# Kernel tuning notes

Measured on AMD Instinct MI355X. Metric: run time of the kernel, lower is better.

The kernel has to match this reference:

```python
import jax, jax.numpy as jnp
import numpy as np

B = 2048
S = 8            # mem_slots
H = 8            # num_heads
HS = 128         # head_size
KS = 128         # key_size (= head_size)
VS = 128         # value_size
M = H * HS       # mem_size = 1024
QKV = 2 * KS + VS            # 384
TOTAL = QKV * H              # 3072
IN_DIM = 1024
NUM_GATES = 2                # gate_style='memory' -> gate size 1, x2 gates
FORGET_BIAS = 1.0
INPUT_BIAS = 0.0


def _glorot(key, shape):
    fan_in, fan_out = shape[0], shape[1]
    lim = np.sqrt(6.0 / (fan_in + fan_out))
    return jax.random.uniform(key, shape, jnp.float32, -lim, lim)


def setup_inputs() -> dict:
    key = jax.random.key(0)
    ks = jax.random.split(key, 16)
    return {
        "inputs": jax.random.normal(ks[0], (B, IN_DIM), jnp.float32),
        "memory": jax.random.normal(ks[1], (B, S * M), jnp.float32),
        "kernel_qkv": _glorot(ks[2], (M, TOTAL)),
        "bias_qkv": jnp.zeros((TOTAL,), jnp.float32),
        "kernel_gi": _glorot(ks[3], (M, NUM_GATES)),
        "bias_gi": _glorot(ks[4], (1, NUM_GATES))[0],
        "kernel_gm": _glorot(ks[5], (M, NUM_GATES)),
        "bias_gm": _glorot(ks[6], (1, NUM_GATES))[0],
        "kernel_in": _glorot(ks[7], (IN_DIM, M)),
        "bias_in": _glorot(ks[8], (1, M))[0],
        "mlp_k0": _glorot(ks[9], (M, M)),
        "mlp_b0": _glorot(ks[10], (1, M))[0],
        "mlp_k1": _glorot(ks[11], (M, M)),
        "mlp_b1": _glorot(ks[12], (1, M))[0],
    }


def reference(inputs, memory, kernel_qkv, bias_qkv, kernel_gi, bias_gi,
              kernel_gm, bias_gm, kernel_in, bias_in,
              mlp_k0, mlp_b0, mlp_k1, mlp_b1):
    b = inputs.shape[0]
    mem = memory.reshape(b, S, M)                       # (B, S, M)
    x = inputs @ kernel_in + bias_in                    # (B, M)
    mpi = jnp.concatenate([mem, x[:, None, :]], axis=1)  # (B, S+1, M)

    # multi-head attention over memory + input slot
    qkv = (mpi @ kernel_qkv + bias_qkv).reshape(b, S + 1, H, QKV)
    qkv = qkv.transpose(0, 2, 1, 3)                     # (B, H, S+1, QKV)
    q = qkv[..., :KS] * (QKV ** -0.5)
    k = qkv[..., KS:2 * KS]
    v = qkv[..., 2 * KS:]
    w = jax.nn.softmax(jnp.einsum('bhqd,bhkd->bhqk', q, k), axis=-1)
    att = jnp.einsum('bhqk,bhkd->bhqd', w, v)           # (B, H, S+1, VS)
    att = att.transpose(0, 2, 1, 3).reshape(b, S + 1, M)
    m1 = mpi + att                                      # residual attention

    # residual 2-layer MLP (relu between layers)
    h = jax.nn.relu(m1 @ mlp_k0 + mlp_b0)
    m2 = m1 + (h @ mlp_k1 + mlp_b1)

    nxt = m2[:, :-1, :]                                 # drop input slot

    # per-slot (memory-style) gates
    gi = (x @ kernel_gi + bias_gi)[:, None, :]          # (B, 1, 2)
    gm = jnp.tanh(mem) @ kernel_gm + bias_gm            # (B, S, 2)
    gates = gm + gi
    input_gate = jax.nn.sigmoid(gates[..., :1] + INPUT_BIAS)
    forget_gate = jax.nn.sigmoid(gates[..., 1:] + FORGET_BIAS)

    nxt = input_gate * jnp.tanh(nxt) + forget_gate * mem
    return nxt.reshape(b, S * M)
```

## Files before the change

kernel.cpp:

```cpp
#include <hip/hip_runtime.h>
#include <math.h>


typedef unsigned short ushort_t;
typedef short bf16x8_t __attribute__((ext_vector_type(8)));
typedef float f32x4_t  __attribute__((ext_vector_type(4)));

#define MFMA16(a, b, c) __builtin_amdgcn_mfma_f32_16x16x32_bf16((a), (b), (c), 0, 0, 0)

__device__ __forceinline__ ushort_t f2bf(float f) {
    unsigned int u = __float_as_uint(f);
    u += 0x7fff + ((u >> 16) & 1);
    return (ushort_t)(u >> 16);
}
__device__ __forceinline__ float bf2f(ushort_t h) {
    return __uint_as_float(((unsigned int)h) << 16);
}
__device__ __forceinline__ float fast_tanh(float x) {
    float e = __expf(2.0f * x);
    return 1.0f - 2.0f * __builtin_amdgcn_rcpf(e + 1.0f);
}
__device__ __forceinline__ float fast_sigmoid(float x) {
    return __builtin_amdgcn_rcpf(1.0f + __expf(-x));
}

__device__ __forceinline__ void load_lds_16(const void* g, void* l) {
    __builtin_amdgcn_global_load_lds(
        (const __attribute__((address_space(1))) void*)g,
        (__attribute__((address_space(3))) void*)l, 16, 0, 0);
}

__global__ __launch_bounds__(256)
void gemm128db(const ushort_t* __restrict__ A, const ushort_t* __restrict__ Wt,
               const float* __restrict__ bias, float* __restrict__ Cf,
               ushort_t* __restrict__ Cb, const ushort_t* __restrict__ resb,
               const float* __restrict__ igfg, const ushort_t* __restrict__ memb,
               float* __restrict__ outp, int N, int K, int relu,
               int ncol, int nrow)
{
    __shared__ __align__(16) ushort_t As[2][128][32];
    __shared__ __align__(16) ushort_t Bs[2][128][32];
    const int tid  = threadIdx.x;
    const int wave = tid >> 6, lane = tid & 63;
    const int wr = (wave >> 1) * 64;
    const int wc = (wave & 1)  * 64;
    const int lrow  = lane & 15;
    const int lquad = lane >> 4;

    int l = blockIdx.x, rT, cT;
    if ((nrow & 7) == 0) {
        int group = l / (8 * ncol);
        int w     = l - group * 8 * ncol;
        rT = group * 8 + (w & 7);
        cT = w >> 3;
    } else {
        rT = l / ncol;
        cT = l - rT * ncol;
    }
    const int rowBase = rT * 128;
    const int colBase = cT * 128;

    auto stage = [&](const ushort_t* __restrict__ G, int gbase, int k0,
                     ushort_t (*lds)[32]) {
        #pragma unroll
        for (int i = 0; i < 2; ++i) {
            int e   = i * 256 + tid;
            int row = e >> 2;
            int sl  = e & 3;
            int gc  = sl ^ ((row >> 1) & 3);
            const ushort_t* g = G + (size_t)(gbase + row) * K + k0 + gc * 8;
            load_lds_16(g, &lds[row][sl * 8]);
        }
    };

    f32x4_t acc[4][4] = {};

    stage(A,  rowBase, 0, As[0]);
    stage(Wt, colBase, 0, Bs[0]);
    __syncthreads();

    int buf = 0;
    for (int k0 = 0; k0 < K; k0 += 32) {
        if (k0 + 32 < K) {
            stage(A,  rowBase, k0 + 32, As[buf ^ 1]);
            stage(Wt, colBase, k0 + 32, Bs[buf ^ 1]);
        }

        bf16x8_t af[4], bfr[4];
        #pragma unroll
        for (int t = 0; t < 4; ++t) {
            int ma = wr + t * 16 + lrow;
            int pa = lquad ^ ((ma >> 1) & 3);
            af[t]  = *(const bf16x8_t*)&As[buf][ma][pa * 8];
            int nb = wc + t * 16 + lrow;
            int pb = lquad ^ ((nb >> 1) & 3);
            bfr[t] = *(const bf16x8_t*)&Bs[buf][nb][pb * 8];
        }
        #pragma unroll
        for (int mi = 0; mi < 4; ++mi)
            #pragma unroll
            for (int ni = 0; ni < 4; ++ni)
                acc[mi][ni] = MFMA16(af[mi], bfr[ni], acc[mi][ni]);

        __syncthreads();
        buf ^= 1;
    }

    #pragma unroll
    for (int mi = 0; mi < 4; ++mi) {
        #pragma unroll
        for (int ni = 0; ni < 4; ++ni) {
            int col = colBase + wc + ni * 16 + lrow;
            float bv = bias[col];
            #pragma unroll
            for (int r = 0; r < 4; ++r) {
                int row = rowBase + wr + mi * 16 + lquad * 4 + r;
                size_t idx = (size_t)row * N + col;
                float v = acc[mi][ni][r] + bv;
                if (resb) v += bf2f(resb[idx]);
                if (relu) v = fmaxf(v, 0.f);
                if (outp) {
                    float ig = igfg[row * 2], fg = igfg[row * 2 + 1];
                    float mv = bf2f(memb[(size_t)(row + (row >> 3)) * N + col]);
                    outp[idx] = ig * fast_tanh(v) + fg * mv;
                } else if (Cb) {
                    Cb[idx] = f2bf(v);
                } else {
                    Cf[idx] = v;
                }
            }
        }
    }
}

__global__ __launch_bounds__(512, 2)
void gemm256(const ushort_t* __restrict__ A, const ushort_t* __restrict__ Wt,
             const float* __restrict__ bias, ushort_t* __restrict__ Cb,
             int N, int K, int ncol, int nrow)
{
    __shared__ __align__(16) ushort_t As[2][256][64];
    __shared__ __align__(16) ushort_t Bs[2][256][64];

    const int tid   = threadIdx.x;
    const int wave  = tid >> 6, lane = tid & 63;
    const int lrow  = lane & 15, lquad = lane >> 4;
    const int wr    = (wave >> 2) * 64;
    const int wc    = (wave & 3) * 32;

    const int nwg = ncol * nrow;
    int l = blockIdx.x;
    int q = nwg >> 3, r = nwg & 7;
    int xcd = l & 7, ib = l >> 3;
    int wg = (xcd < r) ? xcd * (q + 1) + ib : r * (q + 1) + (xcd - r) * q + ib;
    int rT = wg / ncol, cT = wg - rT * ncol;
    const int rowBase = rT * 256;
    const int colBase = cT * 256;

    const int NT = K >> 6;

    auto stage = [&](const ushort_t* __restrict__ G, int gbase, int kt,
                     int half, ushort_t (*lds)[64]) {
        #pragma unroll
        for (int j = 0; j < 2; ++j) {
            int ci   = j * 512 + tid;
            int rl   = ci >> 3;
            int slot = ci & 7;
            int row  = half * 128 + rl;
            int gc   = slot ^ (rl & 7);
            const ushort_t* g = G + (size_t)(gbase + row) * K + kt * 64 + gc * 8;
            load_lds_16(g, &lds[row][slot * 8]);
        }
    };

    stage(A,  rowBase, 0, 0, As[0]);
    stage(A,  rowBase, 0, 1, As[0]);
    stage(Wt, colBase, 0, 0, Bs[0]);
    stage(Wt, colBase, 0, 1, Bs[0]);
    asm volatile("" ::: "memory");
    stage(A,  rowBase, 1, 0, As[1]);
    stage(Wt, colBase, 1, 0, Bs[1]);
    asm volatile("s_waitcnt vmcnt(4)" ::: "memory");
    __builtin_amdgcn_s_barrier();

    f32x4_t acc[8][4] = {};
    bf16x8_t af[4][2], bfr[4][2];
    const int s0 = (lquad ^ (lrow & 7)) * 8;
    const int s1 = ((lquad ^ (lrow & 7)) ^ 4) * 8;

    for (int t = 0; t < NT; ++t) {
        const int bf = t & 1, nf = bf ^ 1;
        ushort_t (*Ab)[64] = As[bf];
        ushort_t (*Bb)[64] = Bs[bf];

        #pragma unroll
        for (int m = 0; m < 4; ++m) {
            int ra = wr + m * 16 + lrow;
            af[m][0] = *(const bf16x8_t*)&Ab[ra][s0];
            af[m][1] = *(const bf16x8_t*)&Ab[ra][s1];
        }
        #pragma unroll
        for (int n = 0; n < 2; ++n) {
            int rb = wc + n * 16 + lrow;
            bfr[n][0] = *(const bf16x8_t*)&Bb[rb][s0];
            bfr[n][1] = *(const bf16x8_t*)&Bb[rb][s1];
        }
        if (t + 1 < NT) stage(A, rowBase, t + 1, 1, As[nf]);
        __builtin_amdgcn_s_barrier();
        asm volatile("s_waitcnt lgkmcnt(0)" ::: "memory");
        __builtin_amdgcn_s_setprio(1);
        #pragma unroll
        for (int m = 0; m < 4; ++m)
            #pragma unroll
            for (int n = 0; n < 2; ++n) {
                acc[m][n] = MFMA16(af[m][0], bfr[n][0], acc[m][n]);
                acc[m][n] = MFMA16(af[m][1], bfr[n][1], acc[m][n]);
            }
        __builtin_amdgcn_s_setprio(0);
        __builtin_amdgcn_s_barrier();

        #pragma unroll
        for (int n = 0; n < 2; ++n) {
            int rb = 128 + wc + n * 16 + lrow;
            bfr[2 + n][0] = *(const bf16x8_t*)&Bb[rb][s0];
            bfr[2 + n][1] = *(const bf16x8_t*)&Bb[rb][s1];
        }
        if (t + 1 < NT) stage(Wt, colBase, t + 1, 1, Bs[nf]);
        __builtin_amdgcn_s_barrier();
        asm volatile("s_waitcnt lgkmcnt(0)" ::: "memory");
        __builtin_amdgcn_s_setprio(1);
        #pragma unroll
        for (int m = 0; m < 4; ++m)
            #pragma unroll
            for (int n = 0; n < 2; ++n) {
                acc[m][2 + n] = MFMA16(af[m][0], bfr[2 + n][0], acc[m][2 + n]);
                acc[m][2 + n] = MFMA16(af[m][1], bfr[2 + n][1], acc[m][2 + n]);
            }
        __builtin_amdgcn_s_setprio(0);
        __builtin_amdgcn_s_barrier();

        #pragma unroll
        for (int m = 0; m < 4; ++m) {
            int ra = 128 + wr + m * 16 + lrow;
            af[m][0] = *(const bf16x8_t*)&Ab[ra][s0];
            af[m][1] = *(const bf16x8_t*)&Ab[ra][s1];
        }
        if (t + 2 < NT) stage(A, rowBase, t + 2, 0, As[bf]);
        __builtin_amdgcn_s_barrier();
        asm volatile("s_waitcnt lgkmcnt(0)" ::: "memory");
        __builtin_amdgcn_s_setprio(1);
        #pragma unroll
        for (int m = 0; m < 4; ++m)
            #pragma unroll
            for (int n = 0; n < 2; ++n) {
                acc[4 + m][n] = MFMA16(af[m][0], bfr[n][0], acc[4 + m][n]);
                acc[4 + m][n] = MFMA16(af[m][1], bfr[n][1], acc[4 + m][n]);
            }
        __builtin_amdgcn_s_setprio(0);
        __builtin_amdgcn_s_barrier();

        if (t + 2 < NT) {
            stage(Wt, colBase, t + 2, 0, Bs[bf]);
            asm volatile("s_waitcnt vmcnt(4)" ::: "memory");
        } else if (t + 1 < NT) {
            asm volatile("s_waitcnt vmcnt(0)" ::: "memory");
        }
        __builtin_amdgcn_s_barrier();
        __builtin_amdgcn_s_setprio(1);
        #pragma unroll
        for (int m = 0; m < 4; ++m)
            #pragma unroll
            for (int n = 0; n < 2; ++n) {
                acc[4 + m][2 + n] = MFMA16(af[m][0], bfr[2 + n][0], acc[4 + m][2 + n]);
                acc[4 + m][2 + n] = MFMA16(af[m][1], bfr[2 + n][1], acc[4 + m][2 + n]);
            }
        __builtin_amdgcn_s_setprio(0);
        __builtin_amdgcn_s_barrier();
    }

    #pragma unroll
    for (int mi = 0; mi < 8; ++mi) {
        #pragma unroll
        for (int ni = 0; ni < 4; ++ni) {
            int col = colBase + wc + (ni & 1) * 16 + ((ni >> 1) << 7) + lrow;
            float bv = bias[col];
            #pragma unroll
            for (int rr = 0; rr < 4; ++rr) {
                int row = rowBase + wr + (mi & 3) * 16 + ((mi >> 2) << 7)
                        + lquad * 4 + rr;
                size_t idx = (size_t)row * N + col;
                Cb[idx] = f2bf(acc[mi][ni][rr] + bv);
            }
        }
    }
}

__global__ __launch_bounds__(256)
void conv_bf16(const float* __restrict__ in, ushort_t* __restrict__ out, size_t n)
{
    size_t i = ((size_t)blockIdx.x * 256 + threadIdx.x) * 4;
    if (i >= n) return;
    float4 v = *(const float4*)(in + i);
    out[i + 0] = f2bf(v.x); out[i + 1] = f2bf(v.y);
    out[i + 2] = f2bf(v.z); out[i + 3] = f2bf(v.w);
}

__global__ __launch_bounds__(256)
void conv_wt4(const float* __restrict__ W0, ushort_t* __restrict__ T0,
              const float* __restrict__ W1, ushort_t* __restrict__ T1,
              const float* __restrict__ W2, ushort_t* __restrict__ T2,
              const float* __restrict__ W3, ushort_t* __restrict__ T3)
{
    __shared__ float t[32][33];
    int bx = blockIdx.x;
    const float* W; ushort_t* T; int N;
    if (bx < 32)       { W = W0; T = T0; N = 1024; }
    else if (bx < 128) { W = W1; T = T1; N = 3072; bx -= 32; }
    else if (bx < 160) { W = W2; T = T2; N = 1024; bx -= 128; }
    else               { W = W3; T = T3; N = 1024; bx -= 160; }
    const int K = 1024;
    const int n0 = bx * 32, k0 = blockIdx.y * 32;
    const int tx = threadIdx.x & 31, ty = threadIdx.x >> 5;
    #pragma unroll
    for (int i = 0; i < 4; ++i)
        t[ty * 4 + i][tx] = W[(size_t)(k0 + ty * 4 + i) * N + n0 + tx];
    __syncthreads();
    #pragma unroll
    for (int i = 0; i < 4; ++i)
        T[(size_t)(n0 + ty * 4 + i) * K + k0 + tx] = f2bf(t[tx][ty * 4 + i]);
}

__global__ __launch_bounds__(256)
void prep_kernel(const float* __restrict__ mem, const ushort_t* __restrict__ xb,
                 const float* __restrict__ kgm, const float* __restrict__ bgm,
                 const float* __restrict__ gi, ushort_t* __restrict__ mpi,
                 float* __restrict__ igfg)
{
    const int row = blockIdx.x;
    const int tid = threadIdx.x;
    const int b = row / 9, s = row - b * 9;
    if (s == 8) {
        ((ushort4*)(mpi + (size_t)row * 1024))[tid] =
            ((const ushort4*)(xb + (size_t)b * 1024))[tid];
        return;
    }
    const float* mrow = mem + ((size_t)b * 8 + s) * 1024;
    float4 v = ((const float4*)mrow)[tid];
    ushort4 o;
    o.x = f2bf(v.x); o.y = f2bf(v.y); o.z = f2bf(v.z); o.w = f2bf(v.w);
    ((ushort4*)(mpi + (size_t)row * 1024))[tid] = o;
    float4 k0 = ((const float4*)kgm)[tid * 2];
    float4 k1 = ((const float4*)kgm)[tid * 2 + 1];
    float t0 = fast_tanh(v.x), t1 = fast_tanh(v.y);
    float t2 = fast_tanh(v.z), t3 = fast_tanh(v.w);
    float g0 = t0 * k0.x + t1 * k0.z + t2 * k1.x + t3 * k1.z;
    float g1 = t0 * k0.y + t1 * k0.w + t2 * k1.y + t3 * k1.w;
    #pragma unroll
    for (int m = 1; m <= 32; m <<= 1) {
        g0 += __shfl_xor(g0, m);
        g1 += __shfl_xor(g1, m);
    }
    __shared__ float wg[4][2];
    if ((tid & 63) == 0) { wg[tid >> 6][0] = g0; wg[tid >> 6][1] = g1; }
    __syncthreads();
    if (tid == 0) {
        float G0 = wg[0][0] + wg[1][0] + wg[2][0] + wg[3][0];
        float G1 = wg[0][1] + wg[1][1] + wg[2][1] + wg[3][1];
        int orow = b * 8 + s;
        igfg[orow * 2 + 0] = fast_sigmoid(G0 + bgm[0] + gi[b * 2 + 0]);
        igfg[orow * 2 + 1] = fast_sigmoid(G1 + bgm[1] + gi[b * 2 + 1] + 1.0f);
    }
}

__global__ __launch_bounds__(256)
void attn_kernel(const ushort_t* __restrict__ qkv, const ushort_t* __restrict__ mpib,
                 ushort_t* __restrict__ m1b)
{
    const int bh = blockIdx.x;
    const int b = bh >> 3, h = bh & 7;
    constexpr int VS = 40;
    __shared__ __align__(16) ushort_t vt[128 * VS];
    __shared__ __align__(16) ushort_t pw[16 * VS];
    const int tid  = threadIdx.x;
    const int lane = tid & 63, wave = tid >> 6;
    const int quad = lane >> 4;
    const size_t qrow0 = (size_t)b * 9;

    {
        unsigned long long* z = (unsigned long long*)vt;
        #pragma unroll
        for (int i = 0; i < 5; ++i) z[tid + i * 256] = 0ull;
        if (tid < 160) ((unsigned long long*)pw)[tid] = 0ull;
    }
    __syncthreads();
    for (int c = tid; c < 9 * 128; c += 256) {
        int j = c >> 7, d = c & 127;
        vt[d * VS + j] = qkv[(qrow0 + j) * 3072 + (size_t)h * 384 + 256 + d];
    }

    f32x4_t sacc = {0.f, 0.f, 0.f, 0.f};
    if (wave == 0) {
        const int m  = lane & 7;
        const int n  = lane & 15;
        const int nc = n > 8 ? 8 : n;
        const ushort_t* qb = qkv + (qrow0 + m)  * 3072 + (size_t)h * 384 + quad * 8;
        const ushort_t* kb = qkv + (qrow0 + nc) * 3072 + (size_t)h * 384 + 128 + quad * 8;
        #pragma unroll
        for (int t = 0; t < 4; ++t) {
            bf16x8_t aq = *(const bf16x8_t*)(qb + t * 32);
            bf16x8_t bk = *(const bf16x8_t*)(kb + t * 32);
            sacc = __builtin_amdgcn_mfma_f32_16x16x32_bf16(aq, bk, sacc, 0, 0, 0);
        }
    }
    __syncthreads();

    if (wave == 0) {
        const int j = lane & 15;
        const float scale = 0.05103103630798288f;
        #pragma unroll
        for (int r = 0; r < 4; ++r) {
            float sv = (j < 9) ? sacc[r] * scale : -1e30f;
            float mx = sv;
            mx = fmaxf(mx, __shfl_xor(mx, 1));
            mx = fmaxf(mx, __shfl_xor(mx, 2));
            mx = fmaxf(mx, __shfl_xor(mx, 4));
            mx = fmaxf(mx, __shfl_xor(mx, 8));
            float e = (j < 9) ? __expf(sv - mx) : 0.f;
            float sum = e;
            sum += __shfl_xor(sum, 1);
            sum += __shfl_xor(sum, 2);
            sum += __shfl_xor(sum, 4);
            sum += __shfl_xor(sum, 8);
            pw[(quad * 4 + r) * VS + j] = f2bf(e * __builtin_amdgcn_rcpf(sum));
        }
    }
    __syncthreads();

    {
        const int n  = lane & 15;
        const int d0 = wave * 32;
        bf16x8_t pa = *(const bf16x8_t*)&pw[n * VS + quad * 8];
        #pragma unroll
        for (int g = 0; g < 2; ++g) {
            int d = d0 + g * 16 + n;
            bf16x8_t vb = *(const bf16x8_t*)&vt[d * VS + quad * 8];
            f32x4_t o = {0.f, 0.f, 0.f, 0.f};
            o = __builtin_amdgcn_mfma_f32_16x16x32_bf16(pa, vb, o, 0, 0, 0);
            #pragma unroll
            for (int r = 0; r < 4; ++r) {
                int i = quad * 4 + r;
                if (i < 8) {
                    float mv = bf2f(mpib[((size_t)b * 9 + i) * 1024 + (size_t)h * 128 + d]);
                    size_t idx = ((size_t)b * 8 + i) * 1024 + (size_t)h * 128 + d;
                    m1b[idx] = f2bf(o[r] + mv);
                }
            }
        }
    }
}

__global__ __launch_bounds__(256)
void gi_kernel(const ushort_t* __restrict__ xb, const float* __restrict__ kgi,
               const float* __restrict__ bgi, float* __restrict__ gi)
{
    const int b = blockIdx.x, tid = threadIdx.x;
    float g0 = 0.f, g1 = 0.f;
    for (int k = tid; k < 1024; k += 256) {
        float xv = bf2f(xb[(size_t)b * 1024 + k]);
        g0 += xv * kgi[k * 2];
        g1 += xv * kgi[k * 2 + 1];
    }
    #pragma unroll
    for (int m = 1; m <= 32; m <<= 1) {
        g0 += __shfl_xor(g0, m);
        g1 += __shfl_xor(g1, m);
    }
    __shared__ float wg[4][2];
    if ((tid & 63) == 0) { wg[tid >> 6][0] = g0; wg[tid >> 6][1] = g1; }
    __syncthreads();
    if (tid == 0) {
        gi[b * 2 + 0] = wg[0][0] + wg[1][0] + wg[2][0] + wg[3][0] + bgi[0];
        gi[b * 2 + 1] = wg[0][1] + wg[1][1] + wg[2][1] + wg[3][1] + bgi[1];
    }
}

extern "C" void kernel_launch(void* const* d_in, const int* in_sizes, int n_in,
                              void* d_out, int out_size, void* d_ws, size_t ws_size,
                              hipStream_t stream)
{
    const float* inputs     = (const float*)d_in[0];
    const float* memory     = (const float*)d_in[1];
    const float* kernel_qkv = (const float*)d_in[2];
    const float* bias_qkv   = (const float*)d_in[3];
    const float* kernel_gi  = (const float*)d_in[4];
    const float* bias_gi    = (const float*)d_in[5];
    const float* kernel_gm  = (const float*)d_in[6];
    const float* bias_gm    = (const float*)d_in[7];
    const float* kernel_in  = (const float*)d_in[8];
    const float* bias_in    = (const float*)d_in[9];
    const float* mlp_k0     = (const float*)d_in[10];
    const float* mlp_b0     = (const float*)d_in[11];
    const float* mlp_k1     = (const float*)d_in[12];
    const float* mlp_b1     = (const float*)d_in[13];
    float* out = (float*)d_out;

    char* p = (char*)d_ws;
    ushort_t* in_b   = (ushort_t*)p;  p += (size_t)2048 * 1024 * 2;
    ushort_t* x_b    = (ushort_t*)p;  p += (size_t)2048 * 1024 * 2;
    ushort_t* wt_in  = (ushort_t*)p;  p += (size_t)1024 * 1024 * 2;
    ushort_t* wt_qkv = (ushort_t*)p;  p += (size_t)3072 * 1024 * 2;
    ushort_t* wt_k0  = (ushort_t*)p;  p += (size_t)1024 * 1024 * 2;
    ushort_t* wt_k1  = (ushort_t*)p;  p += (size_t)1024 * 1024 * 2;
    float*    ws_gi  = (float*)p;     p += (size_t)2048 * 2 * 4;
    float*    igfg   = (float*)p;     p += (size_t)16384 * 2 * 4;
    ushort_t* ws_mpi = (ushort_t*)p;  p += (size_t)18432 * 1024 * 2;
    ushort_t* m1b    = (ushort_t*)p;  p += (size_t)16384 * 1024 * 2;
    ushort_t* ws_h   = (ushort_t*)p;  p += (size_t)16384 * 1024 * 2;
    size_t fixed = (size_t)(p - (char*)d_ws);

    int Bc = 256;
    for (int cand = 1024; cand >= 256; cand >>= 1)
        if (fixed + (size_t)cand * 9 * 3072 * 2 <= ws_size) { Bc = cand; break; }
    ushort_t* ws_qkv = (ushort_t*)p;

    conv_bf16<<<2048, 256, 0, stream>>>(inputs, in_b, (size_t)2048 * 1024);
    conv_wt4<<<dim3(192, 32), 256, 0, stream>>>(
        kernel_in, wt_in, kernel_qkv, wt_qkv, mlp_k0, wt_k0, mlp_k1, wt_k1);

    gemm128db<<<16 * 8, 256, 0, stream>>>(
        in_b, wt_in, bias_in, nullptr, x_b, nullptr, nullptr, nullptr, nullptr,
        1024, 1024, 0, 8, 16);

    gi_kernel<<<2048, 256, 0, stream>>>(x_b, kernel_gi, bias_gi, ws_gi);
    prep_kernel<<<18432, 256, 0, stream>>>(memory, x_b, kernel_gm, bias_gm,
                                           ws_gi, ws_mpi, igfg);

    const int NC = 2048 / Bc;
    for (int c = 0; c < NC; ++c) {
        const int b0 = c * Bc;
        const int nrow = Bc * 9 / 256;
        gemm256<<<12 * nrow, 512, 0, stream>>>(
            ws_mpi + (size_t)b0 * 9 * 1024, wt_qkv, bias_qkv, ws_qkv,
            3072, 1024, 12, nrow);
        attn_kernel<<<Bc * 8, 256, 0, stream>>>(
            ws_qkv, ws_mpi + (size_t)b0 * 9 * 1024, m1b + (size_t)b0 * 8192);
    }

    gemm128db<<<128 * 8, 256, 0, stream>>>(
        m1b, wt_k0, mlp_b0, nullptr, ws_h, nullptr, nullptr, nullptr, nullptr,
        1024, 1024, 1, 8, 128);

    gemm128db<<<128 * 8, 256, 0, stream>>>(
        ws_h, wt_k1, mlp_b1, nullptr, nullptr, m1b, igfg, ws_mpi, out,
        1024, 1024, 0, 8, 128);
}
```

Before: 550.7 us.

## Make 128x128 GEMM stage per-wave LDS tiles without block barriers

Restructures the 128x128 bf16 GEMM so that each wave loads its own 64-row A and B slabs into a private LDS region. It then synchronises only with vmcnt/lgkmcnt waits, dropping the block-wide __syncthreads. Prefetch distance grows to two k-tiles, and launch bounds request two blocks per CU. The cost is redundant global loads, since each wave fetches A and B rows that a neighbouring wave also uses. LDS usage rises to 64KB per block, which may limit occupancy.

```diff
diff --git a/kernel.cpp b/kernel.cpp
--- a/kernel.cpp
+++ b/kernel.cpp
@@ -30,22 +30,21 @@
         (__attribute__((address_space(3))) void*)l, 16, 0, 0);
 }
 
-__global__ __launch_bounds__(256)
-void gemm128db(const ushort_t* __restrict__ A, const ushort_t* __restrict__ Wt,
-               const float* __restrict__ bias, float* __restrict__ Cf,
-               ushort_t* __restrict__ Cb, const ushort_t* __restrict__ resb,
-               const float* __restrict__ igfg, const ushort_t* __restrict__ memb,
-               float* __restrict__ outp, int N, int K, int relu,
-               int ncol, int nrow)
-{
-    __shared__ __align__(16) ushort_t As[2][128][32];
-    __shared__ __align__(16) ushort_t Bs[2][128][32];
+__global__ __launch_bounds__(256, 2)
+void gemm128w(const ushort_t* __restrict__ A, const ushort_t* __restrict__ Wt,
+              const float* __restrict__ bias, float* __restrict__ Cf,
+              ushort_t* __restrict__ Cb, const ushort_t* __restrict__ resb,
+              const float* __restrict__ igfg, const ushort_t* __restrict__ memb,
+              float* __restrict__ outp, int N, int K, int relu,
+              int ncol, int nrow)
+{
+    __shared__ __align__(16) ushort_t lds[4][2][2][64][32];
     const int tid  = threadIdx.x;
     const int wave = tid >> 6, lane = tid & 63;
+    const int lrow  = lane & 15;
+    const int lquad = lane >> 4;
     const int wr = (wave >> 1) * 64;
     const int wc = (wave & 1)  * 64;
-    const int lrow  = lane & 15;
-    const int lquad = lane >> 4;
 
     int l = blockIdx.x, rT, cT;
     if ((nrow & 7) == 0) {
@@ -60,50 +59,63 @@
     const int rowBase = rT * 128;
     const int colBase = cT * 128;
 
-    auto stage = [&](const ushort_t* __restrict__ G, int gbase, int k0,
-                     ushort_t (*lds)[32]) {
-        #pragma unroll
-        for (int i = 0; i < 2; ++i) {
-            int e   = i * 256 + tid;
-            int row = e >> 2;
-            int sl  = e & 3;
-            int gc  = sl ^ ((row >> 1) & 3);
-            const ushort_t* g = G + (size_t)(gbase + row) * K + k0 + gc * 8;
-            load_lds_16(g, &lds[row][sl * 8]);
+    const ushort_t* srcA[4];
+    const ushort_t* srcB[4];
+    #pragma unroll
+    for (int i = 0; i < 4; ++i) {
+        int c   = i * 64 + lane;
+        int row = c >> 2, slot = c & 3;
+        int gc  = slot ^ ((row >> 1) & 3);
+        srcA[i] = A  + (size_t)(rowBase + wr + row) * K + gc * 8;
+        srcB[i] = Wt + (size_t)(colBase + wc + row) * K + gc * 8;
+    }
+
+    auto stageW = [&](int k0, int b) {
+        #pragma unroll
+        for (int i = 0; i < 4; ++i) {
+            int c   = i * 64 + lane;
+            int row = c >> 2, slot = c & 3;
+            load_lds_16(srcA[i] + k0, &lds[wave][b][0][row][slot * 8]);
+        }
+        #pragma unroll
+        for (int i = 0; i < 4; ++i) {
+            int c   = i * 64 + lane;
+            int row = c >> 2, slot = c & 3;
+            load_lds_16(srcB[i] + k0, &lds[wave][b][1][row][slot * 8]);
         }
     };
 
+    const int NT = K >> 5;
+
+    stageW(0,  0);
+    stageW(32, 1);
+
     f32x4_t acc[4][4] = {};
 
-    stage(A,  rowBase, 0, As[0]);
-    stage(Wt, colBase, 0, Bs[0]);
-    __syncthreads();
-
-    int buf = 0;
-    for (int k0 = 0; k0 < K; k0 += 32) {
-        if (k0 + 32 < K) {
-            stage(A,  rowBase, k0 + 32, As[buf ^ 1]);
-            stage(Wt, colBase, k0 + 32, Bs[buf ^ 1]);
-        }
+    for (int t = 0; t < NT; ++t) {
+        const int b = t & 1;
+        if (t + 1 < NT)
+            asm volatile("s_waitcnt vmcnt(8)" ::: "memory");
+        else
+            asm volatile("s_waitcnt vmcnt(0)" ::: "memory");
 
         bf16x8_t af[4], bfr[4];
         #pragma unroll
-        for (int t = 0; t < 4; ++t) {
-            int ma = wr + t * 16 + lrow;
-            int pa = lquad ^ ((ma >> 1) & 3);
-            af[t]  = *(const bf16x8_t*)&As[buf][ma][pa * 8];
-            int nb = wc + t * 16 + lrow;
-            int pb = lquad ^ ((nb >> 1) & 3);
-            bfr[t] = *(const bf16x8_t*)&Bs[buf][nb][pb * 8];
-        }
+        for (int q = 0; q < 4; ++q) {
+            int ra = q * 16 + lrow;
+            int pa = lquad ^ ((ra >> 1) & 3);
+            af[q]  = *(const bf16x8_t*)&lds[wave][b][0][ra][pa * 8];
+            bfr[q] = *(const bf16x8_t*)&lds[wave][b][1][ra][pa * 8];
+        }
+        asm volatile("s_waitcnt lgkmcnt(0)" ::: "memory");
+        __builtin_amdgcn_sched_barrier(0);
+        if (t + 2 < NT) stageW((t + 2) * 32, b);
+
         #pragma unroll
         for (int mi = 0; mi < 4; ++mi)
             #pragma unroll
             for (int ni = 0; ni < 4; ++ni)
                 acc[mi][ni] = MFMA16(af[mi], bfr[ni], acc[mi][ni]);
-
-        __syncthreads();
-        buf ^= 1;
     }
 
     #pragma unroll
@@ -526,7 +538,7 @@
     conv_wt4<<<dim3(192, 32), 256, 0, stream>>>(
         kernel_in, wt_in, kernel_qkv, wt_qkv, mlp_k0, wt_k0, mlp_k1, wt_k1);
 
-    gemm128db<<<16 * 8, 256, 0, stream>>>(
+    gemm128w<<<16 * 8, 256, 0, stream>>>(
         in_b, wt_in, bias_in, nullptr, x_b, nullptr, nullptr, nullptr, nullptr,
         1024, 1024, 0, 8, 16);
 
@@ -545,11 +557,11 @@
             ws_qkv, ws_mpi + (size_t)b0 * 9 * 1024, m1b + (size_t)b0 * 8192);
     }
 
-    gemm128db<<<128 * 8, 256, 0, stream>>>(
+    gemm128w<<<128 * 8, 256, 0, stream>>>(
         m1b, wt_k0, mlp_b0, nullptr, ws_h, nullptr, nullptr, nullptr, nullptr,
         1024, 1024, 1, 8, 128);
 
-    gemm128db<<<128 * 8, 256, 0, stream>>>(
+    gemm128w<<<128 * 8, 256, 0, stream>>>(
         ws_h, wt_k1, mlp_b1, nullptr, nullptr, m1b, igfg, ws_mpi, out,
         1024, 1024, 0, 8, 128);
 }
```

Result: no change. 555.8 us (+0.9%).

## Replace LDS-staged GEMM with direct-from-global register double-buffered loads

Applied to the files above, without the earlier changes.

The 128x128 GEMM used for the input projection and both MLP layers no longer stages A and B tiles through shared memory with barriers. Each wave now loads its own MFMA fragments straight from global memory into registers, with two register sets ping-ponged across k-steps, and the launch bounds request three blocks per CU. This removes LDS traffic and __syncthreads. In exchange the two waves sharing a row or column tile both fetch it from global memory, leaning on cache, and each lane's 16-byte loads are strided by K rather than coalesced.

```diff
diff --git a/kernel.cpp b/kernel.cpp
--- a/kernel.cpp
+++ b/kernel.cpp
@@ -30,22 +30,20 @@
         (__attribute__((address_space(3))) void*)l, 16, 0, 0);
 }
 
-__global__ __launch_bounds__(256)
-void gemm128db(const ushort_t* __restrict__ A, const ushort_t* __restrict__ Wt,
-               const float* __restrict__ bias, float* __restrict__ Cf,
-               ushort_t* __restrict__ Cb, const ushort_t* __restrict__ resb,
-               const float* __restrict__ igfg, const ushort_t* __restrict__ memb,
-               float* __restrict__ outp, int N, int K, int relu,
-               int ncol, int nrow)
-{
-    __shared__ __align__(16) ushort_t As[2][128][32];
-    __shared__ __align__(16) ushort_t Bs[2][128][32];
+__global__ __launch_bounds__(256, 3)
+void gemm128r(const ushort_t* __restrict__ A, const ushort_t* __restrict__ Wt,
+              const float* __restrict__ bias, float* __restrict__ Cf,
+              ushort_t* __restrict__ Cb, const ushort_t* __restrict__ resb,
+              const float* __restrict__ igfg, const ushort_t* __restrict__ memb,
+              float* __restrict__ outp, int N, int K, int relu,
+              int ncol, int nrow)
+{
     const int tid  = threadIdx.x;
     const int wave = tid >> 6, lane = tid & 63;
+    const int lrow  = lane & 15;
+    const int lquad = lane >> 4;
     const int wr = (wave >> 1) * 64;
     const int wc = (wave & 1)  * 64;
-    const int lrow  = lane & 15;
-    const int lquad = lane >> 4;
 
     int l = blockIdx.x, rT, cT;
     if ((nrow & 7) == 0) {
@@ -60,50 +58,37 @@
     const int rowBase = rT * 128;
     const int colBase = cT * 128;
 
-    auto stage = [&](const ushort_t* __restrict__ G, int gbase, int k0,
-                     ushort_t (*lds)[32]) {
-        #pragma unroll
-        for (int i = 0; i < 2; ++i) {
-            int e   = i * 256 + tid;
-            int row = e >> 2;
-            int sl  = e & 3;
-            int gc  = sl ^ ((row >> 1) & 3);
-            const ushort_t* g = G + (size_t)(gbase + row) * K + k0 + gc * 8;
-            load_lds_16(g, &lds[row][sl * 8]);
-        }
+    const ushort_t* pa = A  + (size_t)(rowBase + wr + lrow) * K + lquad * 8;
+    const ushort_t* pb = Wt + (size_t)(colBase + wc + lrow) * K + lquad * 8;
+
+    auto LD = [&](bf16x8_t* d, const ushort_t* base, int k) {
+        #pragma unroll
+        for (int m = 0; m < 4; ++m)
+            d[m] = *(const bf16x8_t*)(base + (size_t)m * 16 * K + k);
     };
 
     f32x4_t acc[4][4] = {};
-
-    stage(A,  rowBase, 0, As[0]);
-    stage(Wt, colBase, 0, Bs[0]);
-    __syncthreads();
-
-    int buf = 0;
-    for (int k0 = 0; k0 < K; k0 += 32) {
-        if (k0 + 32 < K) {
-            stage(A,  rowBase, k0 + 32, As[buf ^ 1]);
-            stage(Wt, colBase, k0 + 32, Bs[buf ^ 1]);
-        }
-
-        bf16x8_t af[4], bfr[4];
-        #pragma unroll
-        for (int t = 0; t < 4; ++t) {
-            int ma = wr + t * 16 + lrow;
-            int pa = lquad ^ ((ma >> 1) & 3);
-            af[t]  = *(const bf16x8_t*)&As[buf][ma][pa * 8];
-            int nb = wc + t * 16 + lrow;
-            int pb = lquad ^ ((nb >> 1) & 3);
-            bfr[t] = *(const bf16x8_t*)&Bs[buf][nb][pb * 8];
-        }
+    bf16x8_t a0[4], b0[4], a1[4], b1[4];
+
+    LD(a0, pa, 0);
+    LD(b0, pb, 0);
+    for (int k0 = 0; k0 < K; k0 += 64) {
+        LD(a1, pa, k0 + 32);
+        LD(b1, pb, k0 + 32);
         #pragma unroll
         for (int mi = 0; mi < 4; ++mi)
             #pragma unroll
             for (int ni = 0; ni < 4; ++ni)
-                acc[mi][ni] = MFMA16(af[mi], bfr[ni], acc[mi][ni]);
-
-        __syncthreads();
-        buf ^= 1;
+                acc[mi][ni] = MFMA16(a0[mi], b0[ni], acc[mi][ni]);
+        if (k0 + 64 < K) {
+            LD(a0, pa, k0 + 64);
+            LD(b0, pb, k0 + 64);
+        }
+        #pragma unroll
+        for (int mi = 0; mi < 4; ++mi)
+            #pragma unroll
+            for (int ni = 0; ni < 4; ++ni)
+                acc[mi][ni] = MFMA16(a1[mi], b1[ni], acc[mi][ni]);
     }
 
     #pragma unroll
@@ -526,7 +511,7 @@
     conv_wt4<<<dim3(192, 32), 256, 0, stream>>>(
         kernel_in, wt_in, kernel_qkv, wt_qkv, mlp_k0, wt_k0, mlp_k1, wt_k1);
 
-    gemm128db<<<16 * 8, 256, 0, stream>>>(
+    gemm128r<<<16 * 8, 256, 0, stream>>>(
         in_b, wt_in, bias_in, nullptr, x_b, nullptr, nullptr, nullptr, nullptr,
         1024, 1024, 0, 8, 16);
 
@@ -545,11 +530,11 @@
             ws_qkv, ws_mpi + (size_t)b0 * 9 * 1024, m1b + (size_t)b0 * 8192);
     }
 
-    gemm128db<<<128 * 8, 256, 0, stream>>>(
+    gemm128r<<<128 * 8, 256, 0, stream>>>(
         m1b, wt_k0, mlp_b0, nullptr, ws_h, nullptr, nullptr, nullptr, nullptr,
         1024, 1024, 1, 8, 128);
 
-    gemm128db<<<128 * 8, 256, 0, stream>>>(
+    gemm128r<<<128 * 8, 256, 0, stream>>>(
         ws_h, wt_k1, mlp_b1, nullptr, nullptr, m1b, igfg, ws_mpi, out,
         1024, 1024, 0, 8, 128);
 }
```

After: 706.9 us. 1.28x slower.

## Fuse two-layer MLP into one kernel keeping hidden activations in LDS

Applied to the files above, without the earlier changes.

Replaces the two separate MLP GEMM launches with a single kernel. Each block processes 32 rows, computes the relu hidden layer into shared memory, then runs the second GEMM plus the gated output epilogue from it. This removes the global write and read of the hidden tensor and one launch. In exchange, each block re-streams both full weight matrices with small 32-row tiles and no double buffering, which greatly raises weight traffic and lowers MFMA intensity.

```diff
diff --git a/kernel.cpp b/kernel.cpp
--- a/kernel.cpp
+++ b/kernel.cpp
@@ -30,13 +30,132 @@
         (__attribute__((address_space(3))) void*)l, 16, 0, 0);
 }
 
+__global__ __launch_bounds__(256, 2)
+void mlp_fused(const ushort_t* __restrict__ m1, const ushort_t* __restrict__ k0t,
+               const float* __restrict__ b0, const ushort_t* __restrict__ k1t,
+               const float* __restrict__ b1, const float* __restrict__ igfg,
+               const ushort_t* __restrict__ memb, float* __restrict__ out)
+{
+    __shared__ __align__(16) ushort_t hs[32][1024];
+    __shared__ __align__(16) ushort_t As[32][32];
+    __shared__ __align__(16) ushort_t Bs[128][32];
+    const int tid   = threadIdx.x;
+    const int wave  = tid >> 6, lane = tid & 63;
+    const int lrow  = lane & 15, lquad = lane >> 4;
+    const int rowBase = blockIdx.x * 32;
+
+    for (int p = 0; p < 8; ++p) {
+        f32x4_t acc[2][2] = {};
+        for (int kk = 0; kk < 32; ++kk) {
+            const int kOff = kk * 32;
+            if (tid < 128) {
+                int row = tid >> 2, sl = tid & 3;
+                int gc  = sl ^ ((row >> 1) & 3);
+                load_lds_16(m1 + (size_t)(rowBase + row) * 1024 + kOff + gc * 8,
+                            &As[row][sl * 8]);
+            }
+            #pragma unroll
+            for (int i = 0; i < 2; ++i) {
+                int e = i * 256 + tid, row = e >> 2, sl = e & 3;
+                int gc = sl ^ ((row >> 1) & 3);
+                load_lds_16(k0t + (size_t)(p * 128 + row) * 1024 + kOff + gc * 8,
+                            &Bs[row][sl * 8]);
+            }
+            __syncthreads();
+            bf16x8_t af[2], bfr[2];
+            #pragma unroll
+            for (int m = 0; m < 2; ++m) {
+                int ma = m * 16 + lrow, pa = lquad ^ ((ma >> 1) & 3);
+                af[m] = *(const bf16x8_t*)&As[ma][pa * 8];
+            }
+            #pragma unroll
+            for (int n = 0; n < 2; ++n) {
+                int nb = wave * 32 + n * 16 + lrow, pb = lquad ^ ((nb >> 1) & 3);
+                bfr[n] = *(const bf16x8_t*)&Bs[nb][pb * 8];
+            }
+            #pragma unroll
+            for (int m = 0; m < 2; ++m)
+                #pragma unroll
+                for (int n = 0; n < 2; ++n)
+                    acc[m][n] = MFMA16(af[m], bfr[n], acc[m][n]);
+            __syncthreads();
+        }
+        #pragma unroll
+        for (int m = 0; m < 2; ++m) {
+            #pragma unroll
+            for (int n = 0; n < 2; ++n) {
+                int coll = wave * 32 + n * 16 + lrow;
+                float bv = b0[p * 128 + coll];
+                #pragma unroll
+                for (int r = 0; r < 4; ++r) {
+                    int row = m * 16 + lquad * 4 + r;
+                    float v = fmaxf(acc[m][n][r] + bv, 0.f);
+                    int col  = p * 128 + coll;
+                    int ch   = col >> 3;
+                    int phys = ((ch ^ (row & 7)) << 3) + (col & 7);
+                    hs[row][phys] = f2bf(v);
+                }
+            }
+        }
+        __syncthreads();
+    }
+
+    for (int p = 0; p < 8; ++p) {
+        f32x4_t acc[2][2] = {};
+        for (int kk = 0; kk < 32; ++kk) {
+            const int kOff = kk * 32;
+            #pragma unroll
+            for (int i = 0; i < 2; ++i) {
+                int e = i * 256 + tid, row = e >> 2, sl = e & 3;
+                int gc = sl ^ ((row >> 1) & 3);
+                load_lds_16(k1t + (size_t)(p * 128 + row) * 1024 + kOff + gc * 8,
+                            &Bs[row][sl * 8]);
+            }
+            __syncthreads();
+            bf16x8_t af[2], bfr[2];
+            #pragma unroll
+            for (int m = 0; m < 2; ++m) {
+                int row  = m * 16 + lrow;
+                int ch   = kk * 4 + lquad;
+                int phys = ((ch ^ (row & 7)) << 3);
+                af[m] = *(const bf16x8_t*)&hs[row][phys];
+            }
+            #pragma unroll
+            for (int n = 0; n < 2; ++n) {
+                int nb = wave * 32 + n * 16 + lrow, pb = lquad ^ ((nb >> 1) & 3);
+                bfr[n] = *(const bf16x8_t*)&Bs[nb][pb * 8];
+            }
+            #pragma unroll
+            for (int m = 0; m < 2; ++m)
+                #pragma unroll
+                for (int n = 0; n < 2; ++n)
+                    acc[m][n] = MFMA16(af[m], bfr[n], acc[m][n]);
+            __syncthreads();
+        }
+        #pragma unroll
+        for (int m = 0; m < 2; ++m) {
+            #pragma unroll
+            for (int n = 0; n < 2; ++n) {
+                int col = p * 128 + wave * 32 + n * 16 + lrow;
+                float bv = b1[col];
+                #pragma unroll
+                for (int r = 0; r < 4; ++r) {
+                    int row = rowBase + m * 16 + lquad * 4 + r;
+                    size_t idx = (size_t)row * 1024 + col;
+                    float v = acc[m][n][r] + bv + bf2f(m1[idx]);
+                    float ig = igfg[row * 2], fg = igfg[row * 2 + 1];
+                    float mv = bf2f(memb[(size_t)(row + (row >> 3)) * 1024 + col]);
+                    out[idx] = ig * fast_tanh(v) + fg * mv;
+                }
+            }
+        }
+    }
+}
+
 __global__ __launch_bounds__(256)
 void gemm128db(const ushort_t* __restrict__ A, const ushort_t* __restrict__ Wt,
-               const float* __restrict__ bias, float* __restrict__ Cf,
-               ushort_t* __restrict__ Cb, const ushort_t* __restrict__ resb,
-               const float* __restrict__ igfg, const ushort_t* __restrict__ memb,
-               float* __restrict__ outp, int N, int K, int relu,
-               int ncol, int nrow)
+               const float* __restrict__ bias, ushort_t* __restrict__ Cb,
+               int N, int K, int ncol, int nrow)
 {
     __shared__ __align__(16) ushort_t As[2][128][32];
     __shared__ __align__(16) ushort_t Bs[2][128][32];
@@ -85,7 +204,6 @@
             stage(A,  rowBase, k0 + 32, As[buf ^ 1]);
             stage(Wt, colBase, k0 + 32, Bs[buf ^ 1]);
         }
-
         bf16x8_t af[4], bfr[4];
         #pragma unroll
         for (int t = 0; t < 4; ++t) {
@@ -101,7 +219,6 @@
             #pragma unroll
             for (int ni = 0; ni < 4; ++ni)
                 acc[mi][ni] = MFMA16(af[mi], bfr[ni], acc[mi][ni]);
-
         __syncthreads();
         buf ^= 1;
     }
@@ -115,19 +232,7 @@
             #pragma unroll
             for (int r = 0; r < 4; ++r) {
                 int row = rowBase + wr + mi * 16 + lquad * 4 + r;
-                size_t idx = (size_t)row * N + col;
-                float v = acc[mi][ni][r] + bv;
-                if (resb) v += bf2f(resb[idx]);
-                if (relu) v = fmaxf(v, 0.f);
-                if (outp) {
-                    float ig = igfg[row * 2], fg = igfg[row * 2 + 1];
-                    float mv = bf2f(memb[(size_t)(row + (row >> 3)) * N + col]);
-                    outp[idx] = ig * fast_tanh(v) + fg * mv;
-                } else if (Cb) {
-                    Cb[idx] = f2bf(v);
-                } else {
-                    Cf[idx] = v;
-                }
+                Cb[(size_t)row * N + col] = f2bf(acc[mi][ni][r] + bv);
             }
         }
     }
@@ -514,7 +619,6 @@
     float*    igfg   = (float*)p;     p += (size_t)16384 * 2 * 4;
     ushort_t* ws_mpi = (ushort_t*)p;  p += (size_t)18432 * 1024 * 2;
     ushort_t* m1b    = (ushort_t*)p;  p += (size_t)16384 * 1024 * 2;
-    ushort_t* ws_h   = (ushort_t*)p;  p += (size_t)16384 * 1024 * 2;
     size_t fixed = (size_t)(p - (char*)d_ws);
 
     int Bc = 256;
@@ -527,8 +631,7 @@
         kernel_in, wt_in, kernel_qkv, wt_qkv, mlp_k0, wt_k0, mlp_k1, wt_k1);
 
     gemm128db<<<16 * 8, 256, 0, stream>>>(
-        in_b, wt_in, bias_in, nullptr, x_b, nullptr, nullptr, nullptr, nullptr,
-        1024, 1024, 0, 8, 16);
+        in_b, wt_in, bias_in, x_b, 1024, 1024, 8, 16);
 
     gi_kernel<<<2048, 256, 0, stream>>>(x_b, kernel_gi, bias_gi, ws_gi);
     prep_kernel<<<18432, 256, 0, stream>>>(memory, x_b, kernel_gm, bias_gm,
@@ -545,11 +648,6 @@
             ws_qkv, ws_mpi + (size_t)b0 * 9 * 1024, m1b + (size_t)b0 * 8192);
     }
 
-    gemm128db<<<128 * 8, 256, 0, stream>>>(
-        m1b, wt_k0, mlp_b0, nullptr, ws_h, nullptr, nullptr, nullptr, nullptr,
-        1024, 1024, 1, 8, 128);
-
-    gemm128db<<<128 * 8, 256, 0, stream>>>(
-        ws_h, wt_k1, mlp_b1, nullptr, nullptr, m1b, igfg, ws_mpi, out,
-        1024, 1024, 0, 8, 128);
-}
+    mlp_fused<<<512, 256, 0, stream>>>(
+        m1b, wt_k0, mlp_b0, wt_k1, mlp_b1, igfg, ws_mpi, out);
+}
```

Measured after the change: 584.7 us. 1.06x slower.
